# Performance work log

Measured on AMD Instinct MI355X. Metric: run time of the kernel, lower is better.

Reference implementation:

```python
import jax, jax.numpy as jnp
import numpy as np

EPS = 1e-6
B, I, N, Wd, R = 128, 512, 512, 32, 4


def setup_inputs() -> dict:
    key = jax.random.key(0)
    ks = jax.random.split(key, 32)
    inp = {
        "xi": jax.random.normal(ks[0], (B, I), jnp.float32),
        "memory": jax.random.normal(ks[1], (B, N, Wd), jnp.float32),
        "link_matrix": jax.random.uniform(ks[2], (B, N, N), jnp.float32),
        "precedence": jax.random.uniform(ks[3], (B, N), jnp.float32),
        "read_weights": jax.random.uniform(ks[4], (B, R, N), jnp.float32),
        "write_weights": jax.random.uniform(ks[5], (B, N), jnp.float32),
        "usage": jax.random.uniform(ks[6], (B, N), jnp.float32),
    }
    # 10 independent linear heads (weight [out, in], bias [out]) as in independent_linears=True
    dims = [("rk", R * Wd), ("rs", R), ("wk", Wd), ("ws", 1), ("ev", Wd),
            ("wv", Wd), ("fg", R), ("ag", 1), ("wg", 1), ("rm", 3 * R)]
    scale = 1.0 / np.sqrt(I).astype(np.float32)
    for i, (nm, d) in enumerate(dims):
        inp["W_" + nm] = jax.random.normal(ks[7 + 2 * i], (d, I), jnp.float32) * scale
        inp["b_" + nm] = jax.random.normal(ks[8 + 2 * i], (d,), jnp.float32) * 0.01
    return inp


def reference(xi, memory, link_matrix, precedence, read_weights, write_weights, usage,
              W_rk, b_rk, W_rs, b_rs, W_wk, b_wk, W_ws, b_ws, W_ev, b_ev,
              W_wv, b_wv, W_fg, b_fg, W_ag, b_ag, W_wg, b_wg, W_rm, b_rm):
    b, n, w = memory.shape
    r = b_rs.shape[0]
    lin = lambda Wm, bm: xi @ Wm.T + bm

    # interface vectors
    read_keys = jnp.tanh(lin(W_rk, b_rk)).reshape(b, r, w)          # [B,R,W]
    read_str = jax.nn.softplus(lin(W_rs, b_rs))                      # [B,R]
    write_key = jnp.tanh(lin(W_wk, b_wk))                            # [B,W]
    write_str = jax.nn.softplus(lin(W_ws, b_ws))                     # [B,1]
    erase = jax.nn.sigmoid(lin(W_ev, b_ev))                          # [B,W]
    write_vec = jnp.tanh(lin(W_wv, b_wv))                            # [B,W]
    free = jax.nn.sigmoid(lin(W_fg, b_fg))                           # [B,R]
    alloc_g = jax.nn.sigmoid(lin(W_ag, b_ag))                        # [B,1]
    write_g = jax.nn.sigmoid(lin(W_wg, b_wg))                        # [B,1]
    modes = jax.nn.softmax(lin(W_rm, b_rm).reshape(b, r, 3), axis=2)

    # usage update (memory retention)
    psi = jnp.prod(1.0 - free[:, :, None] * read_weights, axis=1)    # [B,N]
    usage = (usage + write_weights - usage * write_weights) * psi

    # allocation weighting via sorted usage
    idx = jnp.argsort(usage, axis=1)
    su = jnp.take_along_axis(usage, idx, axis=1)
    prod_excl = jnp.concatenate(
        [jnp.ones((b, 1), su.dtype), jnp.cumprod(su, axis=1)[:, :-1]], axis=1)
    alloc_sorted = (1.0 - su) * prod_excl
    alloc = jnp.zeros_like(usage).at[jnp.arange(b)[:, None], idx].set(alloc_sorted)

    # write content addressing (cosine similarity)
    mem_norm = jnp.linalg.norm(memory, axis=2)                       # [B,N]
    wsim = jnp.einsum('bnw,bw->bn', memory, write_key) / (
        mem_norm * jnp.linalg.norm(write_key, axis=1, keepdims=True) + EPS)
    wc = jax.nn.softmax(write_str * wsim, axis=1)                    # [B,N]

    ww = write_g * (alloc_g * alloc + (1.0 - alloc_g) * wc)          # [B,N]

    # memory write (erase then add)
    memory = memory * (1.0 - ww[:, :, None] * erase[:, None, :]) \
             + ww[:, :, None] * write_vec[:, None, :]

    # temporal link matrix + precedence update
    link = (1.0 - ww[:, :, None] - ww[:, None, :]) * link_matrix \
           + ww[:, :, None] * precedence[:, None, :]
    link = link * (1.0 - jnp.eye(n, dtype=link.dtype))
    precedence = (1.0 - jnp.sum(ww, axis=1, keepdims=True)) * precedence + ww

    # directional read weights from previous read weights
    fw = jnp.einsum('bnm,brm->brn', link, read_weights)              # forward: L w
    bw = jnp.einsum('bmn,brm->brn', link, read_weights)              # backward: L^T w

    # read content addressing on updated memory
    mem_norm2 = jnp.linalg.norm(memory, axis=2)
    rsim = jnp.einsum('bnw,brw->brn', memory, read_keys) / (
        mem_norm2[:, None, :] * jnp.linalg.norm(read_keys, axis=2, keepdims=True) + EPS)
    rc = jax.nn.softmax(read_str[:, :, None] * rsim, axis=2)         # [B,R,N]

    read_weights = modes[:, :, 0:1] * bw + modes[:, :, 1:2] * rc + modes[:, :, 2:3] * fw
    read_vectors = jnp.einsum('brn,bnw->brw', read_weights, memory)  # [B,R,W]
    return read_vectors, memory, link, precedence, read_weights, ww, usage
```

## Files before the change

### kernel.cpp

```cpp
#include <hip/hip_runtime.h>
#include <math.h>

#define BB 128
#define ID 512
#define NN 512
#define WDIM 32
#define RR 4
#define EPSF 1e-6f
#define NTILE 16

typedef float nt_float4 __attribute__((ext_vector_type(4)));

#define OFF_RV   ((size_t)0)
#define OFF_MEM  (OFF_RV + (size_t)BB*RR*WDIM)
#define OFF_LINK (OFF_MEM + (size_t)BB*NN*WDIM)
#define OFF_PREC (OFF_LINK + (size_t)BB*NN*NN)
#define OFF_RW   (OFF_PREC + (size_t)BB*NN)
#define OFF_WW   (OFF_RW + (size_t)BB*RR*NN)
#define OFF_USG  (OFF_WW + (size_t)BB*NN)

#define IF_RK 0
#define IF_RS 128
#define IF_WK 132
#define IF_WS 164
#define IF_EV 165
#define IF_WV 197
#define IF_FG 229
#define IF_AG 233
#define IF_WG 234
#define IF_RM 235

#define WS_IFACE ((size_t)0)
#define WS_FW    (WS_IFACE + (size_t)BB*256)
#define WS_BW    (WS_FW + (size_t)BB*RR*NN)

__device__ __forceinline__ float sigm(float x) { return 1.0f / (1.0f + expf(-x)); }
__device__ __forceinline__ float softplusf(float x) { return fmaxf(x, 0.0f) + log1pf(expf(-fabsf(x))); }

struct HeadArgs {
  const float *Wrk, *brk, *Wrs, *brs, *Wwk, *bwk, *Wws, *bws, *Wev, *bev,
              *Wwv, *bwv, *Wfg, *bfg, *Wag, *bag, *Wwg, *bwg, *Wrm, *brm;
};

__global__ __launch_bounds__(256) void k1_heads(const float* __restrict__ xi, HeadArgs ha,
                                                float* __restrict__ iface) {
  __shared__ __align__(16) float xs[ID];
  __shared__ float raw[256];
  int b = blockIdx.x, t = threadIdx.x;
  for (int i = t; i < ID; i += 256) xs[i] = xi[b * ID + i];
  __syncthreads();
  const float* Ws[10] = {ha.Wrk, ha.Wrs, ha.Wwk, ha.Wws, ha.Wev, ha.Wwv, ha.Wfg, ha.Wag, ha.Wwg, ha.Wrm};
  const float* bs[10] = {ha.brk, ha.brs, ha.bwk, ha.bws, ha.bev, ha.bwv, ha.bfg, ha.bag, ha.bwg, ha.brm};
  const int off[11] = {0, 128, 132, 164, 165, 197, 229, 233, 234, 235, 247};
  float val = 0.0f;
  int h = -1, row = 0;
  if (t < 247) {
    for (int k = 0; k < 10; ++k)
      if (t >= off[k] && t < off[k + 1]) { h = k; row = t - off[k]; }
    const float4* w4 = (const float4*)(Ws[h] + row * ID);
    const float4* x4 = (const float4*)xs;
    float acc = 0.0f;
    for (int i = 0; i < ID / 4; ++i) {
      float4 w = w4[i], x = x4[i];
      acc += w.x * x.x + w.y * x.y + w.z * x.z + w.w * x.w;
    }
    val = acc + bs[h][row];
  }
  raw[t] = val;
  __syncthreads();
  if (t < 247) {
    float o;
    if (h == 0 || h == 2 || h == 5) o = tanhf(val);
    else if (h == 1 || h == 3) o = softplusf(val);
    else if (h == 9) {
      int g = (t - 235) / 3;
      float a0 = raw[235 + g * 3], a1 = raw[236 + g * 3], a2 = raw[237 + g * 3];
      float mx = fmaxf(a0, fmaxf(a1, a2));
      o = expf(val - mx) / (expf(a0 - mx) + expf(a1 - mx) + expf(a2 - mx));
    } else o = sigm(val);
    iface[b * 256 + t] = o;
  }
}

__global__ __launch_bounds__(512) void k2_write(const float* __restrict__ mem_in,
                                                const float* __restrict__ prec_in,
                                                const float* __restrict__ rw_in,
                                                const float* __restrict__ wwt_in,
                                                const float* __restrict__ usg_in,
                                                const float* __restrict__ iface,
                                                float* __restrict__ bw,
                                                float* __restrict__ out) {
  __shared__ __align__(16) float sif[256];
  __shared__ float sv[NN];
  __shared__ int si[NN];
  __shared__ float salloc[NN];
  __shared__ float sred[8];
  __shared__ float swt[8];
  int b = blockIdx.x, tid = threadIdx.x;
  int lane = tid & 63, wave = tid >> 6;

  for (int i = tid; i < RR * NN; i += 512) bw[(size_t)b * RR * NN + i] = 0.0f;

  if (tid < 256) sif[tid] = iface[b * 256 + tid];
  __syncthreads();

  const float* rwb = rw_in + (size_t)b * RR * NN;
  float psi = 1.0f;
#pragma unroll
  for (int r = 0; r < RR; r++) psi *= 1.0f - sif[IF_FG + r] * rwb[r * NN + tid];
  float u = usg_in[b * NN + tid], wwt = wwt_in[b * NN + tid];
  u = (u + wwt - u * wwt) * psi;

  float v = u; int idx = tid;
  for (int k = 2; k <= NN; k <<= 1) {
    for (int j = k >> 1; j > 0; j >>= 1) {
      int p = tid ^ j;
      float pv; int pi;
      if (j >= 64) {
        sv[tid] = v; si[tid] = idx;
        __syncthreads();
        pv = sv[p]; pi = si[p];
        __syncthreads();
      } else {
        pv = __shfl_xor(v, j);
        pi = __shfl_xor(idx, j);
      }
      bool mineSmaller = (v < pv) || (v == pv && idx < pi);
      bool keepMin = (((tid & k) == 0) == (tid < p));
      bool take = keepMin ? !mineSmaller : mineSmaller;
      if (take) { v = pv; idx = pi; }
    }
  }

  float pr = v;
#pragma unroll
  for (int o = 1; o < 64; o <<= 1) {
    float q = __shfl_up(pr, o);
    if (lane >= o) pr *= q;
  }
  if (lane == 63) swt[wave] = pr;
  __syncthreads();
  float wp = 1.0f;
#pragma unroll
  for (int w = 0; w < 8; w++) if (w < wave) wp *= swt[w];
  float ep = __shfl_up(pr, 1);
  if (lane == 0) ep = 1.0f;
  float alloc_sorted = (1.0f - v) * (wp * ep);
  salloc[idx] = alloc_sorted;
  __syncthreads();
  float alloc = salloc[tid];

  const float4* mrow = (const float4*)(mem_in + ((size_t)b * NN + tid) * WDIM);
  float4 mv[8];
  float dot = 0, nrm = 0, wkn = 0;
#pragma unroll
  for (int i = 0; i < 8; i++) {
    float4 m = mrow[i];
    mv[i] = m;
    const float4 kk = *(const float4*)&sif[IF_WK + 4 * i];
    dot += m.x * kk.x + m.y * kk.y + m.z * kk.z + m.w * kk.w;
    nrm += m.x * m.x + m.y * m.y + m.z * m.z + m.w * m.w;
    wkn += kk.x * kk.x + kk.y * kk.y + kk.z * kk.z + kk.w * kk.w;
  }
  float s = sif[IF_WS] * (dot / (sqrtf(nrm) * sqrtf(wkn) + EPSF));

  float m8 = s;
#pragma unroll
  for (int d = 32; d > 0; d >>= 1) m8 = fmaxf(m8, __shfl_down(m8, d));
  if (lane == 0) sred[wave] = m8;
  __syncthreads();
  float mx = sred[0];
#pragma unroll
  for (int w = 1; w < 8; w++) mx = fmaxf(mx, sred[w]);
  __syncthreads();
  float e = expf(s - mx);
  float sm = e;
#pragma unroll
  for (int d = 32; d > 0; d >>= 1) sm += __shfl_down(sm, d);
  if (lane == 0) sred[wave] = sm;
  __syncthreads();
  float esum = 0;
#pragma unroll
  for (int w = 0; w < 8; w++) esum += sred[w];
  __syncthreads();
  float wc = e / esum;

  float ww = sif[IF_WG] * (sif[IF_AG] * alloc + (1.0f - sif[IF_AG]) * wc);
  out[OFF_WW + b * NN + tid] = ww;
  out[OFF_USG + b * NN + tid] = u;

  float ws_ = ww;
#pragma unroll
  for (int d = 32; d > 0; d >>= 1) ws_ += __shfl_down(ws_, d);
  if (lane == 0) sred[wave] = ws_;
  __syncthreads();
  float wsum = 0;
#pragma unroll
  for (int w = 0; w < 8; w++) wsum += sred[w];
  out[OFF_PREC + b * NN + tid] = (1.0f - wsum) * prec_in[b * NN + tid] + ww;

  float* mo = out + OFF_MEM + ((size_t)b * NN + tid) * WDIM;
#pragma unroll
  for (int i = 0; i < 8; i++) {
    float4 m = mv[i];
    float4 o;
    o.x = m.x * (1.0f - ww * sif[IF_EV + 4 * i + 0]) + ww * sif[IF_WV + 4 * i + 0];
    o.y = m.y * (1.0f - ww * sif[IF_EV + 4 * i + 1]) + ww * sif[IF_WV + 4 * i + 1];
    o.z = m.z * (1.0f - ww * sif[IF_EV + 4 * i + 2]) + ww * sif[IF_WV + 4 * i + 2];
    o.w = m.w * (1.0f - ww * sif[IF_EV + 4 * i + 3]) + ww * sif[IF_WV + 4 * i + 3];
    ((float4*)mo)[i] = o;
  }
}

__global__ __launch_bounds__(256) void k3_link(const float* __restrict__ link_in,
                                               const float* __restrict__ prec_in,
                                               const float* __restrict__ rw_in,
                                               const float* __restrict__ ww_out,
                                               float* __restrict__ link_out,
                                               float* __restrict__ fw,
                                               float* __restrict__ bw) {
  __shared__ __align__(16) float sww[NN];
  __shared__ __align__(16) float sprec[NN];
  __shared__ __align__(16) float srw[RR * NN];
  __shared__ float sbw[RR * NN];
  int b = blockIdx.y, tile = blockIdx.x, tid = threadIdx.x;
  for (int i = tid; i < NN; i += 256) {
    sww[i] = ww_out[b * NN + i];
    sprec[i] = prec_in[b * NN + i];
  }
  for (int i = tid; i < RR * NN; i += 256) {
    srw[i] = rw_in[(size_t)b * RR * NN + i];
    sbw[i] = 0.0f;
  }
  __syncthreads();

  int wave = tid >> 6, lane = tid & 63;
  float4 cww[2], cpr[2], crw[RR][2];
#pragma unroll
  for (int h = 0; h < 2; h++) {
    cww[h] = ((const float4*)sww)[h * 64 + lane];
    cpr[h] = ((const float4*)sprec)[h * 64 + lane];
#pragma unroll
    for (int r = 0; r < RR; r++) crw[r][h] = ((const float4*)(srw + r * NN))[h * 64 + lane];
  }

  float bwa[RR][8];
#pragma unroll
  for (int r = 0; r < RR; r++)
#pragma unroll
    for (int j = 0; j < 8; j++) bwa[r][j] = 0.0f;

  const size_t lbase = (size_t)b * NN * NN;
  const float* lbp = link_in + lbase;
  int row0 = tile * 32 + wave;

  float4 nv0 = ((const float4*)(lbp + (size_t)row0 * NN))[lane];
  float4 nv1 = ((const float4*)(lbp + (size_t)row0 * NN))[64 + lane];

  for (int i = 0; i < 8; i++) {
    int row = row0 + 4 * i;
    float4 cv[2] = {nv0, nv1};
    if (i < 7) {
      const float4* Ln = (const float4*)(lbp + (size_t)(row + 4) * NN);
      nv0 = Ln[lane];
      nv1 = Ln[64 + lane];
    }
    float wwr = sww[row];
    float rwr[RR] = {srw[row], srw[NN + row], srw[2 * NN + row], srw[3 * NN + row]};
    nt_float4* Lo = (nt_float4*)(link_out + lbase + (size_t)row * NN);
    float fp[RR] = {0, 0, 0, 0};
#pragma unroll
    for (int h = 0; h < 2; h++) {
      float4 lv = cv[h];
      float l[4] = {lv.x, lv.y, lv.z, lv.w};
      float wc[4] = {cww[h].x, cww[h].y, cww[h].z, cww[h].w};
      float pc[4] = {cpr[h].x, cpr[h].y, cpr[h].z, cpr[h].w};
      int c0 = h * 256 + 4 * lane;
#pragma unroll
      for (int j = 0; j < 4; j++) {
        float ln = (1.0f - wwr - wc[j]) * l[j] + wwr * pc[j];
        if (c0 + j == row) ln = 0.0f;
        l[j] = ln;
#pragma unroll
        for (int r = 0; r < RR; r++) bwa[r][h * 4 + j] += ln * rwr[r];
      }
#pragma unroll
      for (int r = 0; r < RR; r++) {
        float rc0 = (r == 0) ? crw[0][h].x : (r == 1) ? crw[1][h].x : (r == 2) ? crw[2][h].x : crw[3][h].x;
        float rc1 = (r == 0) ? crw[0][h].y : (r == 1) ? crw[1][h].y : (r == 2) ? crw[2][h].y : crw[3][h].y;
        float rc2 = (r == 0) ? crw[0][h].z : (r == 1) ? crw[1][h].z : (r == 2) ? crw[2][h].z : crw[3][h].z;
        float rc3 = (r == 0) ? crw[0][h].w : (r == 1) ? crw[1][h].w : (r == 2) ? crw[2][h].w : crw[3][h].w;
        fp[r] += l[0] * rc0 + l[1] * rc1 + l[2] * rc2 + l[3] * rc3;
      }
      nt_float4 ov = {l[0], l[1], l[2], l[3]};
      __builtin_nontemporal_store(ov, &Lo[h * 64 + lane]);
    }
#pragma unroll
    for (int d = 32; d > 0; d >>= 1) {
      fp[0] += __shfl_down(fp[0], d);
      fp[1] += __shfl_down(fp[1], d);
      fp[2] += __shfl_down(fp[2], d);
      fp[3] += __shfl_down(fp[3], d);
    }
    if (lane == 0) {
      float* fwb = fw + (size_t)b * RR * NN;
      fwb[0 * NN + row] = fp[0];
      fwb[1 * NN + row] = fp[1];
      fwb[2 * NN + row] = fp[2];
      fwb[3 * NN + row] = fp[3];
    }
  }

  for (int w = 0; w < 4; w++) {
    if (wave == w) {
#pragma unroll
      for (int r = 0; r < RR; r++)
#pragma unroll
        for (int h = 0; h < 2; h++)
#pragma unroll
          for (int j = 0; j < 4; j++)
            sbw[r * NN + h * 256 + 4 * lane + j] += bwa[r][h * 4 + j];
    }
    __syncthreads();
  }
  float* bp = bw + (size_t)b * RR * NN;
  for (int i = tid; i < RR * NN; i += 256) atomicAdd(&bp[i], sbw[i]);
}

__global__ __launch_bounds__(512) void k4_read(const float* __restrict__ iface,
                                               const float* __restrict__ fw,
                                               const float* __restrict__ bw,
                                               float* __restrict__ out) {
  __shared__ __align__(16) float srk[WDIM];
  __shared__ float sred[8];
  __shared__ float srwn[NN];
  __shared__ float spart[16][WDIM];
  int b = blockIdx.x >> 2, r = blockIdx.x & 3;
  int tid = threadIdx.x, lane = tid & 63, wave = tid >> 6;
  const float* ifb = iface + b * 256;
  if (tid < WDIM) srk[tid] = ifb[IF_RK + r * WDIM + tid];
  __syncthreads();
  float rkn2 = 0;
#pragma unroll
  for (int w = 0; w < WDIM; w++) { float v = srk[w]; rkn2 += v * v; }
  float rkn = sqrtf(rkn2);

  const float* mem = out + OFF_MEM + (size_t)b * NN * WDIM;
  const float4* mrow = (const float4*)(mem + (size_t)tid * WDIM);
  float d = 0, nrm = 0;
#pragma unroll
  for (int i = 0; i < 8; i++) {
    float4 m = mrow[i];
    const float4 kk = *(const float4*)&srk[4 * i];
    nrm += m.x * m.x + m.y * m.y + m.z * m.z + m.w * m.w;
    d += m.x * kk.x + m.y * kk.y + m.z * kk.z + m.w * kk.w;
  }
  float s = ifb[IF_RS + r] * (d / (sqrtf(nrm) * rkn + EPSF));

  float m8 = s;
#pragma unroll
  for (int dd = 32; dd > 0; dd >>= 1) m8 = fmaxf(m8, __shfl_down(m8, dd));
  if (lane == 0) sred[wave] = m8;
  __syncthreads();
  float mx = sred[0];
#pragma unroll
  for (int w = 1; w < 8; w++) mx = fmaxf(mx, sred[w]);
  __syncthreads();
  float e = expf(s - mx);
  float sm = e;
#pragma unroll
  for (int dd = 32; dd > 0; dd >>= 1) sm += __shfl_down(sm, dd);
  if (lane == 0) sred[wave] = sm;
  __syncthreads();
  float esum = 0;
#pragma unroll
  for (int w = 0; w < 8; w++) esum += sred[w];
  float rc = e / esum;

  float bwv = bw[((size_t)b * RR + r) * NN + tid];
  float fwv = fw[((size_t)b * RR + r) * NN + tid];
  float m0 = ifb[IF_RM + 3 * r], m1 = ifb[IF_RM + 3 * r + 1], m2 = ifb[IF_RM + 3 * r + 2];
  float v = m0 * bwv + m1 * rc + m2 * fwv;
  srwn[tid] = v;
  out[OFF_RW + ((size_t)b * RR + r) * NN + tid] = v;
  __syncthreads();

  int w = tid & 31, part = tid >> 5;
  float acc = 0;
  const float* mp = mem + (size_t)part * 32 * WDIM + w;
  const float* rp = srwn + part * 32;
#pragma unroll
  for (int n = 0; n < 32; n++) acc += rp[n] * mp[(size_t)n * WDIM];
  spart[part][w] = acc;
  __syncthreads();
  if (tid < WDIM) {
    float vv = 0;
#pragma unroll
    for (int p = 0; p < 16; p++) vv += spart[p][tid];
    out[OFF_RV + ((size_t)b * RR + r) * WDIM + tid] = vv;
  }
}

extern "C" void kernel_launch(void* const* d_in, const int* in_sizes, int n_in,
                              void* d_out, int out_size, void* d_ws, size_t ws_size,
                              hipStream_t stream) {
  const float* xi = (const float*)d_in[0];
  const float* mem = (const float*)d_in[1];
  const float* link = (const float*)d_in[2];
  const float* prec = (const float*)d_in[3];
  const float* rw = (const float*)d_in[4];
  const float* wwt = (const float*)d_in[5];
  const float* usg = (const float*)d_in[6];
  HeadArgs ha;
  ha.Wrk = (const float*)d_in[7];  ha.brk = (const float*)d_in[8];
  ha.Wrs = (const float*)d_in[9];  ha.brs = (const float*)d_in[10];
  ha.Wwk = (const float*)d_in[11]; ha.bwk = (const float*)d_in[12];
  ha.Wws = (const float*)d_in[13]; ha.bws = (const float*)d_in[14];
  ha.Wev = (const float*)d_in[15]; ha.bev = (const float*)d_in[16];
  ha.Wwv = (const float*)d_in[17]; ha.bwv = (const float*)d_in[18];
  ha.Wfg = (const float*)d_in[19]; ha.bfg = (const float*)d_in[20];
  ha.Wag = (const float*)d_in[21]; ha.bag = (const float*)d_in[22];
  ha.Wwg = (const float*)d_in[23]; ha.bwg = (const float*)d_in[24];
  ha.Wrm = (const float*)d_in[25]; ha.brm = (const float*)d_in[26];

  float* out = (float*)d_out;
  float* ws = (float*)d_ws;
  float* iface = ws + WS_IFACE;
  float* fwbuf = ws + WS_FW;
  float* bwbuf = ws + WS_BW;

  k1_heads<<<BB, 256, 0, stream>>>(xi, ha, iface);
  k2_write<<<BB, 512, 0, stream>>>(mem, prec, rw, wwt, usg, iface, bwbuf, out);
  k3_link<<<dim3(NTILE, BB), 256, 0, stream>>>(link, prec, rw, out + OFF_WW, out + OFF_LINK, fwbuf, bwbuf);
  k4_read<<<BB * RR, 512, 0, stream>>>(iface, fwbuf, bwbuf, out);
}
```

Measured before the change: 357.1 us.

## Replace backward-link atomics with per-tile partials and deepen link row prefetch

```diff
diff --git a/kernel.cpp b/kernel.cpp
--- a/kernel.cpp
+++ b/kernel.cpp
@@ -33,6 +33,8 @@
 #define WS_IFACE ((size_t)0)
 #define WS_FW    (WS_IFACE + (size_t)BB*256)
 #define WS_BW    (WS_FW + (size_t)BB*RR*NN)
+#define WS_PART  WS_BW
+#define WS_PART_FLOATS ((size_t)BB*NTILE*RR*NN)
 
 __device__ __forceinline__ float sigm(float x) { return 1.0f / (1.0f + expf(-x)); }
 __device__ __forceinline__ float softplusf(float x) { return fmaxf(x, 0.0f) + log1pf(expf(-fabsf(x))); }
@@ -212,6 +214,7 @@
   }
 }
 
+template<int PARTIAL>
 __global__ __launch_bounds__(256) void k3_link(const float* __restrict__ link_in,
                                                const float* __restrict__ prec_in,
                                                const float* __restrict__ rw_in,
@@ -235,14 +238,11 @@
   __syncthreads();
 
   int wave = tid >> 6, lane = tid & 63;
-  float4 cww[2], cpr[2], crw[RR][2];
-#pragma unroll
-  for (int h = 0; h < 2; h++) {
-    cww[h] = ((const float4*)sww)[h * 64 + lane];
-    cpr[h] = ((const float4*)sprec)[h * 64 + lane];
+  float4 crw[RR][2];
+#pragma unroll
+  for (int h = 0; h < 2; h++)
 #pragma unroll
     for (int r = 0; r < RR; r++) crw[r][h] = ((const float4*)(srw + r * NN))[h * 64 + lane];
-  }
 
   float bwa[RR][8];
 #pragma unroll
@@ -254,16 +254,20 @@
   const float* lbp = link_in + lbase;
   int row0 = tile * 32 + wave;
 
-  float4 nv0 = ((const float4*)(lbp + (size_t)row0 * NN))[lane];
-  float4 nv1 = ((const float4*)(lbp + (size_t)row0 * NN))[64 + lane];
-
+  const float4* La = (const float4*)(lbp + (size_t)row0 * NN);
+  const float4* Lb = (const float4*)(lbp + (size_t)(row0 + 4) * NN);
+  float4 pa0 = La[lane], pa1 = La[64 + lane];
+  float4 pb0 = Lb[lane], pb1 = Lb[64 + lane];
+
+#pragma unroll
   for (int i = 0; i < 8; i++) {
     int row = row0 + 4 * i;
-    float4 cv[2] = {nv0, nv1};
-    if (i < 7) {
-      const float4* Ln = (const float4*)(lbp + (size_t)(row + 4) * NN);
-      nv0 = Ln[lane];
-      nv1 = Ln[64 + lane];
+    float4 cv0, cv1;
+    if ((i & 1) == 0) { cv0 = pa0; cv1 = pa1; } else { cv0 = pb0; cv1 = pb1; }
+    if (i < 6) {
+      const float4* Ln = (const float4*)(lbp + (size_t)(row + 8) * NN);
+      if ((i & 1) == 0) { pa0 = Ln[lane]; pa1 = Ln[64 + lane]; }
+      else { pb0 = Ln[lane]; pb1 = Ln[64 + lane]; }
     }
     float wwr = sww[row];
     float rwr[RR] = {srw[row], srw[NN + row], srw[2 * NN + row], srw[3 * NN + row]};
@@ -271,10 +275,12 @@
     float fp[RR] = {0, 0, 0, 0};
 #pragma unroll
     for (int h = 0; h < 2; h++) {
-      float4 lv = cv[h];
+      float4 lv = (h == 0) ? cv0 : cv1;
+      float4 wq = ((const float4*)sww)[h * 64 + lane];
+      float4 pq = ((const float4*)sprec)[h * 64 + lane];
       float l[4] = {lv.x, lv.y, lv.z, lv.w};
-      float wc[4] = {cww[h].x, cww[h].y, cww[h].z, cww[h].w};
-      float pc[4] = {cpr[h].x, cpr[h].y, cpr[h].z, cpr[h].w};
+      float wc[4] = {wq.x, wq.y, wq.z, wq.w};
+      float pc[4] = {pq.x, pq.y, pq.z, pq.w};
       int c0 = h * 256 + 4 * lane;
 #pragma unroll
       for (int j = 0; j < 4; j++) {
@@ -323,10 +329,16 @@
     }
     __syncthreads();
   }
-  float* bp = bw + (size_t)b * RR * NN;
-  for (int i = tid; i < RR * NN; i += 256) atomicAdd(&bp[i], sbw[i]);
+  if (PARTIAL) {
+    float* bp = bw + ((size_t)(b * NTILE + tile)) * RR * NN;
+    for (int i = tid; i < RR * NN; i += 256) bp[i] = sbw[i];
+  } else {
+    float* bp = bw + (size_t)b * RR * NN;
+    for (int i = tid; i < RR * NN; i += 256) atomicAdd(&bp[i], sbw[i]);
+  }
 }
 
+template<int PARTIAL>
 __global__ __launch_bounds__(512) void k4_read(const float* __restrict__ iface,
                                                const float* __restrict__ fw,
                                                const float* __restrict__ bw,
@@ -377,7 +389,16 @@
   for (int w = 0; w < 8; w++) esum += sred[w];
   float rc = e / esum;
 
-  float bwv = bw[((size_t)b * RR + r) * NN + tid];
+  float bwv;
+  if (PARTIAL) {
+    const float* pp = bw + ((size_t)b * NTILE * RR + r) * NN + tid;
+    float acc = 0.0f;
+#pragma unroll
+    for (int t = 0; t < NTILE; t++) acc += pp[(size_t)t * RR * NN];
+    bwv = acc;
+  } else {
+    bwv = bw[((size_t)b * RR + r) * NN + tid];
+  }
   float fwv = fw[((size_t)b * RR + r) * NN + tid];
   float m0 = ifb[IF_RM + 3 * r], m1 = ifb[IF_RM + 3 * r + 1], m2 = ifb[IF_RM + 3 * r + 2];
   float v = m0 * bwv + m1 * rc + m2 * fwv;
@@ -429,8 +450,16 @@
   float* fwbuf = ws + WS_FW;
   float* bwbuf = ws + WS_BW;
 
+  const size_t need_part_bytes = (WS_PART + WS_PART_FLOATS) * sizeof(float);
+  const bool use_partial = ws_size >= need_part_bytes;
+
   k1_heads<<<BB, 256, 0, stream>>>(xi, ha, iface);
   k2_write<<<BB, 512, 0, stream>>>(mem, prec, rw, wwt, usg, iface, bwbuf, out);
-  k3_link<<<dim3(NTILE, BB), 256, 0, stream>>>(link, prec, rw, out + OFF_WW, out + OFF_LINK, fwbuf, bwbuf);
-  k4_read<<<BB * RR, 512, 0, stream>>>(iface, fwbuf, bwbuf, out);
+  if (use_partial) {
+    k3_link<1><<<dim3(NTILE, BB), 256, 0, stream>>>(link, prec, rw, out + OFF_WW, out + OFF_LINK, fwbuf, ws + WS_PART);
+    k4_read<1><<<BB * RR, 512, 0, stream>>>(iface, fwbuf, ws + WS_PART, out);
+  } else {
+    k3_link<0><<<dim3(NTILE, BB), 256, 0, stream>>>(link, prec, rw, out + OFF_WW, out + OFF_LINK, fwbuf, bwbuf);
+    k4_read<0><<<BB * RR, 512, 0, stream>>>(iface, fwbuf, bwbuf, out);
+  }
 }
```

After: 352.2 us. No clear change (-1.4%).

## Replace backward-read atomics with per-tile partial sums reduced in read kernel

Applied to the files above, without the earlier changes.

```diff
diff --git a/kernel.cpp b/kernel.cpp
--- a/kernel.cpp
+++ b/kernel.cpp
@@ -8,8 +8,6 @@
 #define RR 4
 #define EPSF 1e-6f
 #define NTILE 16
-
-typedef float nt_float4 __attribute__((ext_vector_type(4)));
 
 #define OFF_RV   ((size_t)0)
 #define OFF_MEM  (OFF_RV + (size_t)BB*RR*WDIM)
@@ -33,6 +31,8 @@
 #define WS_IFACE ((size_t)0)
 #define WS_FW    (WS_IFACE + (size_t)BB*256)
 #define WS_BW    (WS_FW + (size_t)BB*RR*NN)
+#define WS_PART  WS_BW
+#define WS_PART_FLOATS ((size_t)BB*NTILE*RR*NN)
 
 __device__ __forceinline__ float sigm(float x) { return 1.0f / (1.0f + expf(-x)); }
 __device__ __forceinline__ float softplusf(float x) { return fmaxf(x, 0.0f) + log1pf(expf(-fabsf(x))); }
@@ -212,6 +212,7 @@
   }
 }
 
+template<int PARTIAL>
 __global__ __launch_bounds__(256) void k3_link(const float* __restrict__ link_in,
                                                const float* __restrict__ prec_in,
                                                const float* __restrict__ rw_in,
@@ -223,6 +224,7 @@
   __shared__ __align__(16) float sprec[NN];
   __shared__ __align__(16) float srw[RR * NN];
   __shared__ float sbw[RR * NN];
+  __shared__ float sfw[RR * 32];
   int b = blockIdx.y, tile = blockIdx.x, tid = threadIdx.x;
   for (int i = tid; i < NN; i += 256) {
     sww[i] = ww_out[b * NN + i];
@@ -267,7 +269,7 @@
     }
     float wwr = sww[row];
     float rwr[RR] = {srw[row], srw[NN + row], srw[2 * NN + row], srw[3 * NN + row]};
-    nt_float4* Lo = (nt_float4*)(link_out + lbase + (size_t)row * NN);
+    float4* Lo = (float4*)(link_out + lbase + (size_t)row * NN);
     float fp[RR] = {0, 0, 0, 0};
 #pragma unroll
     for (int h = 0; h < 2; h++) {
@@ -292,8 +294,8 @@
         float rc3 = (r == 0) ? crw[0][h].w : (r == 1) ? crw[1][h].w : (r == 2) ? crw[2][h].w : crw[3][h].w;
         fp[r] += l[0] * rc0 + l[1] * rc1 + l[2] * rc2 + l[3] * rc3;
       }
-      nt_float4 ov = {l[0], l[1], l[2], l[3]};
-      __builtin_nontemporal_store(ov, &Lo[h * 64 + lane]);
+      float4 ov = {l[0], l[1], l[2], l[3]};
+      Lo[h * 64 + lane] = ov;
     }
 #pragma unroll
     for (int d = 32; d > 0; d >>= 1) {
@@ -303,12 +305,18 @@
       fp[3] += __shfl_down(fp[3], d);
     }
     if (lane == 0) {
-      float* fwb = fw + (size_t)b * RR * NN;
-      fwb[0 * NN + row] = fp[0];
-      fwb[1 * NN + row] = fp[1];
-      fwb[2 * NN + row] = fp[2];
-      fwb[3 * NN + row] = fp[3];
-    }
+      int rl = wave + 4 * i;
+      sfw[0 * 32 + rl] = fp[0];
+      sfw[1 * 32 + rl] = fp[1];
+      sfw[2 * 32 + rl] = fp[2];
+      sfw[3 * 32 + rl] = fp[3];
+    }
+  }
+  __syncthreads();
+
+  if (tid < RR * 32) {
+    int r = tid >> 5, j = tid & 31;
+    fw[(size_t)b * RR * NN + r * NN + tile * 32 + j] = sfw[tid];
   }
 
   for (int w = 0; w < 4; w++) {
@@ -323,10 +331,16 @@
     }
     __syncthreads();
   }
-  float* bp = bw + (size_t)b * RR * NN;
-  for (int i = tid; i < RR * NN; i += 256) atomicAdd(&bp[i], sbw[i]);
+  if (PARTIAL) {
+    float* bp = bw + ((size_t)(b * NTILE + tile)) * RR * NN;
+    for (int i = tid; i < RR * NN; i += 256) bp[i] = sbw[i];
+  } else {
+    float* bp = bw + (size_t)b * RR * NN;
+    for (int i = tid; i < RR * NN; i += 256) atomicAdd(&bp[i], sbw[i]);
+  }
 }
 
+template<int PARTIAL>
 __global__ __launch_bounds__(512) void k4_read(const float* __restrict__ iface,
                                                const float* __restrict__ fw,
                                                const float* __restrict__ bw,
@@ -377,7 +391,16 @@
   for (int w = 0; w < 8; w++) esum += sred[w];
   float rc = e / esum;
 
-  float bwv = bw[((size_t)b * RR + r) * NN + tid];
+  float bwv;
+  if (PARTIAL) {
+    const float* pp = bw + ((size_t)b * NTILE * RR + r) * NN + tid;
+    float acc = 0.0f;
+#pragma unroll
+    for (int t = 0; t < NTILE; t++) acc += pp[(size_t)t * RR * NN];
+    bwv = acc;
+  } else {
+    bwv = bw[((size_t)b * RR + r) * NN + tid];
+  }
   float fwv = fw[((size_t)b * RR + r) * NN + tid];
   float m0 = ifb[IF_RM + 3 * r], m1 = ifb[IF_RM + 3 * r + 1], m2 = ifb[IF_RM + 3 * r + 2];
   float v = m0 * bwv + m1 * rc + m2 * fwv;
@@ -429,8 +452,16 @@
   float* fwbuf = ws + WS_FW;
   float* bwbuf = ws + WS_BW;
 
+  const size_t need_part_bytes = (WS_PART + WS_PART_FLOATS) * sizeof(float);
+  const bool use_partial = ws_size >= need_part_bytes;
+
   k1_heads<<<BB, 256, 0, stream>>>(xi, ha, iface);
   k2_write<<<BB, 512, 0, stream>>>(mem, prec, rw, wwt, usg, iface, bwbuf, out);
-  k3_link<<<dim3(NTILE, BB), 256, 0, stream>>>(link, prec, rw, out + OFF_WW, out + OFF_LINK, fwbuf, bwbuf);
-  k4_read<<<BB * RR, 512, 0, stream>>>(iface, fwbuf, bwbuf, out);
+  if (use_partial) {
+    k3_link<1><<<dim3(NTILE, BB), 256, 0, stream>>>(link, prec, rw, out + OFF_WW, out + OFF_LINK, fwbuf, ws + WS_PART);
+    k4_read<1><<<BB * RR, 512, 0, stream>>>(iface, fwbuf, ws + WS_PART, out);
+  } else {
+    k3_link<0><<<dim3(NTILE, BB), 256, 0, stream>>>(link, prec, rw, out + OFF_WW, out + OFF_LINK, fwbuf, bwbuf);
+    k4_read<0><<<BB * RR, 512, 0, stream>>>(iface, fwbuf, bwbuf, out);
+  }
 }
```

Result: no change. 352.6 us (-1.2%).
